# Kernel tuning notes

Hardware: AMD Instinct MI355X
Metric: run time of the kernel (lower is better)

## Reference

```python
import jax, jax.numpy as jnp
import numpy as np

NUM_EMBEDDINGS = 8192
EMBEDDING_DIM = 512
COMMITMENT_COST = 0.25
DECAY = 0.99
EPSILON = 1e-05


def setup_inputs() -> dict:
    key = jax.random.key(0)
    k1, k2, k3, k4 = jax.random.split(key, 4)
    z = jax.random.normal(k1, (16, 2048, EMBEDDING_DIM), dtype=jnp.float32)
    weight = jax.random.normal(k2, (NUM_EMBEDDINGS, EMBEDDING_DIM), dtype=jnp.float32)
    ema_cluster_size = jax.random.uniform(k3, (NUM_EMBEDDINGS,), dtype=jnp.float32)
    ema_w = jax.random.normal(k4, (NUM_EMBEDDINGS, EMBEDDING_DIM), dtype=jnp.float32)
    return {"z": z, "weight": weight, "ema_cluster_size": ema_cluster_size, "ema_w": ema_w}


def reference(z, weight, ema_cluster_size, ema_w):
    K, D = weight.shape
    z_flat = z.reshape(-1, D)                                   # [N, D]
    # squared-distance matrix via expanded GEMM (same math as torch)
    dist = ((z_flat ** 2).sum(1, keepdims=True)
            + (weight ** 2).sum(1)
            - 2.0 * z_flat @ weight.T)                          # [N, K]
    codes = jnp.argmin(dist, axis=1)                            # [N]
    # training-mode EMA update: one-hot sums expressed as segment_sum
    counts = jax.ops.segment_sum(jnp.ones(z_flat.shape[0], dtype=z.dtype), codes, num_segments=K)
    dw = jax.ops.segment_sum(z_flat, codes, num_segments=K)     # encodings.T @ z_flat
    new_cs = ema_cluster_size * DECAY + (1.0 - DECAY) * counts
    new_ema_w = ema_w * DECAY + (1.0 - DECAY) * dw
    n = new_cs.sum()
    cluster_size = (new_cs + EPSILON) / (n + K * EPSILON) * n
    new_weight = new_ema_w / cluster_size[:, None]              # updated codebook
    z_q = new_weight[codes].reshape(z.shape)                    # lookup with UPDATED weights
    vq_loss = COMMITMENT_COST * jnp.mean((jax.lax.stop_gradient(z_q) - z) ** 2)
    z_q_out = z + jax.lax.stop_gradient(z_q - z)                # straight-through estimator
    codes_out = codes.reshape(z.shape[0], -1)
    return vq_loss, z_q_out, codes_out, new_weight, new_cs, new_ema_w
```

## Files before the change

kernel.cpp:

```cpp
#include <hip/hip_runtime.h>
#include <cstdint>

#define K_CODES 8192
#define D_DIM   512
#define N_VEC   32768
#define DECAY   0.99f
#define EPS_VQ  1e-5f
#define COMMIT  0.25f
#define MARGIN  0.25f

typedef _Float16 half_t;
typedef _Float16 half8 __attribute__((ext_vector_type(8)));
typedef _Float16 half4 __attribute__((ext_vector_type(4)));
typedef float    f32x4 __attribute__((ext_vector_type(4)));
typedef unsigned long long u64;

#define GL2L(g, l)                                                              \
    __builtin_amdgcn_global_load_lds(                                           \
        (const __attribute__((address_space(1))) unsigned int*)(g),             \
        (__attribute__((address_space(3))) unsigned int*)(l), 16, 0, 0)

__device__ __forceinline__ unsigned ordf(float f) {
    unsigned u = __float_as_uint(f);
    return (u & 0x80000000u) ? ~u : (u | 0x80000000u);
}
__device__ __forceinline__ float unordf(unsigned u) {
    u = (u & 0x80000000u) ? (u & 0x7FFFFFFFu) : ~u;
    return __uint_as_float(u);
}


__global__ __launch_bounds__(256)
void conv_half_kernel(const float* __restrict__ x, half_t* __restrict__ out) {
    int i = blockIdx.x * 256 + threadIdx.x;
    float4 v = ((const float4*)x)[i];
    half4 h = { (_Float16)v.x, (_Float16)v.y, (_Float16)v.z, (_Float16)v.w };
    *(half4*)(out + (size_t)i * 4) = h;
}

__global__ __launch_bounds__(256)
void wsq_kernel(const float* __restrict__ w, float* __restrict__ wsq) {
    int wave = threadIdx.x >> 6, lane = threadIdx.x & 63;
    int row  = blockIdx.x * 4 + wave;
    const float4* p = (const float4*)(w + (size_t)row * D_DIM);
    float4 a = p[lane], b = p[lane + 64];
    float s = a.x*a.x + a.y*a.y + a.z*a.z + a.w*a.w
            + b.x*b.x + b.y*b.y + b.z*b.z + b.w*b.w;
    #pragma unroll
    for (int off = 32; off; off >>= 1) s += __shfl_down(s, off);
    if (lane == 0) wsq[row] = s;
}

__global__ __launch_bounds__(256, 4)
void dist1_kernel(const half_t* __restrict__ A, const half_t* __restrict__ B,
                  const float* __restrict__ wsq, uint4* __restrict__ partial) {
    __shared__ __align__(16) char smem[36864];
    half_t* As = (half_t*)smem;
    half_t* Bs = (half_t*)(smem + 16384);

    const int k0 = blockIdx.x * 128;
    const int n0 = blockIdx.y * 128;
    const int t    = threadIdx.x;
    const int lane = t & 63;
    const int wave = t >> 6;
    const int wm = (wave >> 1) * 64;
    const int wn = (wave & 1) * 64;
    const int l15 = lane & 15;
    const int q   = lane >> 4;

    const half_t* ga[4]; const half_t* gb[4]; half_t* lA[4]; half_t* lB[4];
    #pragma unroll
    for (int it = 0; it < 4; ++it) {
        int idx  = t + 256 * it;
        int row  = idx >> 3;
        int col8 = (idx & 7) ^ (row & 7);
        ga[it] = A + (size_t)(n0 + row) * D_DIM + col8 * 8;
        gb[it] = B + (size_t)(k0 + row) * D_DIM + col8 * 8;
        lA[it] = As + idx * 8;
        lB[it] = Bs + idx * 8;
    }

    f32x4 acc[4][4];
    #pragma unroll
    for (int mi = 0; mi < 4; ++mi)
        #pragma unroll
        for (int ni = 0; ni < 4; ++ni) acc[mi][ni] = (f32x4)0.0f;

    #pragma unroll
    for (int c = 0; c < 8; ++c) {
        #pragma unroll
        for (int it = 0; it < 4; ++it) {
            GL2L(ga[it] + c * 64, lA[it]);
            GL2L(gb[it] + c * 64, lB[it]);
        }
        __syncthreads();
        #pragma unroll
        for (int kk = 0; kk < 2; ++kk) {
            half8 af[4], bf[4];
            const int cpos = ((kk * 4 + q) ^ (l15 & 7)) * 8;
            #pragma unroll
            for (int mi = 0; mi < 4; ++mi)
                af[mi] = *(const half8*)&As[(wm + mi * 16 + l15) * 64 + cpos];
            #pragma unroll
            for (int ni = 0; ni < 4; ++ni)
                bf[ni] = *(const half8*)&Bs[(wn + ni * 16 + l15) * 64 + cpos];
            #pragma unroll
            for (int mi = 0; mi < 4; ++mi)
                #pragma unroll
                for (int ni = 0; ni < 4; ++ni)
                    acc[mi][ni] = __builtin_amdgcn_mfma_f32_16x16x32_f16(
                        af[mi], bf[ni], acc[mi][ni], 0, 0, 0);
        }
        __syncthreads();
    }

    uint2* kp  = (uint2*)(smem + wave * 8704);
    uint2* fmp = (uint2*)(smem + 34816);

    float wb[4]; unsigned cb[4];
    #pragma unroll
    for (int ni = 0; ni < 4; ++ni) {
        wb[ni] = 1024.0f - 0.5f * wsq[k0 + wn + ni * 16 + l15];
        cb[ni] = (unsigned)(wn + ni * 16 + l15);
    }

    #pragma unroll
    for (int mi = 0; mi < 4; ++mi) {
        #pragma unroll
        for (int r = 0; r < 4; ++r) {
            unsigned k1 = 0u, k2 = 0u;
            #pragma unroll
            for (int ni = 0; ni < 4; ++ni) {
                float a = acc[mi][ni][r] + wb[ni];
                unsigned key = (__float_as_uint(a) & 0xFFFFFF80u) | cb[ni];
                unsigned lo = min(k1, key);
                k1 = max(k1, key);
                k2 = max(k2, lo);
            }
            int row = mi * 16 + q * 4 + r;
            kp[row * 17 + l15] = make_uint2(k1, k2);
        }
    }
    __syncthreads();

    {
        const int rb = lane * 17;
        uint2 e0 = kp[rb];
        unsigned W1 = e0.x, W2 = e0.y;
        #pragma unroll
        for (int j = 1; j < 16; ++j) {
            uint2 e = kp[rb + j];
            unsigned lo = min(W1, e.x);
            W1 = max(W1, e.x);
            W2 = max(max(W2, lo), e.y);
        }
        fmp[(wave & 1) * 128 + wm + lane] = make_uint2(W1, W2);
    }
    __syncthreads();

    if (t < 128) {
        uint2 a = fmp[t], b = fmp[128 + t];
        unsigned W1 = max(a.x, b.x);
        unsigned W2 = max(max(min(a.x, b.x), a.y), b.y);
        unsigned col = (unsigned)k0 + (W1 & 127u);
        float v1 = __uint_as_float(W1 & 0xFFFFFF80u);
        float v2 = __uint_as_float(W2 & 0xFFFFFF80u);
        float d1 = 2048.0f - 2.0f * v1;
        float d2 = 2048.0f - 2.0f * v2;
        partial[(size_t)blockIdx.x * N_VEC + n0 + t] =
            make_uint4(col, ordf(d1), ordf(d2), 0u);
    }
}

__global__ __launch_bounds__(256)
void reduce_top2_kernel(const uint4* __restrict__ partial,
                        int* __restrict__ codes_i, float* __restrict__ codes_f,
                        int* __restrict__ cnt, int* __restrict__ list) {
    int row = blockIdx.x * 256 + threadIdx.x;
    u64 k1 = ~0ull, k2 = ~0ull;
    unsigned vm2 = 0xFFFFFFFFu;
    for (int kb = 0; kb < 64; ++kb) {
        uint4 e = partial[(size_t)kb * N_VEC + row];
        u64 k = ((u64)e.y << 32) | e.x;
        if (k < k1) { k2 = k1; k1 = k; }
        else if (k < k2) k2 = k;
        vm2 = min(vm2, e.z);
    }
    unsigned so = min((unsigned)(k2 >> 32), vm2);
    float bv = unordf((unsigned)(k1 >> 32));
    float sv = unordf(so);
    int code = (int)(k1 & 0xFFFFFFFFu);
    codes_i[row] = code;
    codes_f[row] = (float)code;
    if (sv - bv < MARGIN) { int p = atomicAdd(cnt, 1); list[p] = row; }
}

__global__ __launch_bounds__(256)
void refine2_kernel(const float* __restrict__ z, const float* __restrict__ w,
                    const float* __restrict__ wsq,
                    const int* __restrict__ cnt, const int* __restrict__ list,
                    u64* __restrict__ exact) {
    __shared__ float zs[64][68];
    __shared__ float ws[64][68];
    __shared__ int rows_s[64];
    const int n  = *cnt;
    const int c0 = blockIdx.x * 64;
    const int t  = threadIdx.x;
    const int lr = t & 63, lc = t >> 6;
    const int ty = t >> 4, tx = t & 15;

    for (int row0 = blockIdx.y * 64; row0 < n; row0 += gridDim.y * 64) {
        if (t < 64) {
            int ri = row0 + t;
            rows_s[t] = list[ri < n ? ri : n - 1];
        }
        __syncthreads();
        float acc[4][4] = {};
        const int zrow = rows_s[lr];
        for (int k0 = 0; k0 < D_DIM; k0 += 64) {
            #pragma unroll
            for (int it = 0; it < 4; ++it) {
                int kc = (lc * 4 + it) * 4;
                float4 v = *(const float4*)(z + (size_t)zrow * D_DIM + k0 + kc);
                zs[kc+0][lr] = v.x; zs[kc+1][lr] = v.y;
                zs[kc+2][lr] = v.z; zs[kc+3][lr] = v.w;
                float4 u = *(const float4*)(w + (size_t)(c0 + lr) * D_DIM + k0 + kc);
                ws[kc+0][lr] = u.x; ws[kc+1][lr] = u.y;
                ws[kc+2][lr] = u.z; ws[kc+3][lr] = u.w;
            }
            __syncthreads();
            #pragma unroll 8
            for (int k = 0; k < 64; ++k) {
                float4 za = *(const float4*)&zs[k][ty * 4];
                float4 wa = *(const float4*)&ws[k][tx * 4];
                float zav[4] = {za.x, za.y, za.z, za.w};
                float wav[4] = {wa.x, wa.y, wa.z, wa.w};
                #pragma unroll
                for (int i = 0; i < 4; ++i)
                    #pragma unroll
                    for (int j = 0; j < 4; ++j)
                        acc[i][j] += zav[i] * wav[j];
            }
            __syncthreads();
        }
        #pragma unroll
        for (int i = 0; i < 4; ++i) {
            u64 key = ~0ull;
            #pragma unroll
            for (int j = 0; j < 4; ++j) {
                int c = c0 + tx * 4 + j;
                float d = wsq[c] - 2.0f * acc[i][j];
                u64 k = ((u64)ordf(d) << 32) | (unsigned)c;
                if (k < key) key = k;
            }
            #pragma unroll
            for (int m = 1; m <= 8; m <<= 1) {
                u64 o = __shfl_xor(key, m);
                key = o < key ? o : key;
            }
            if (tx == 0) atomicMin(exact + rows_s[ty * 4 + i], key);
        }
        __syncthreads();
    }
}

__global__ __launch_bounds__(256)
void refine_fix_kernel(const int* __restrict__ cnt, const int* __restrict__ list,
                       const u64* __restrict__ exact,
                       int* __restrict__ codes_i, float* __restrict__ codes_f) {
    int n = *cnt;
    for (int i = blockIdx.x * 256 + threadIdx.x; i < n; i += 64 * 256) {
        int row = list[i];
        int code = (int)(exact[row] & 0xFFFFFFFFu);
        codes_i[row] = code;
        codes_f[row] = (float)code;
    }
}

__global__ __launch_bounds__(256)
void scatter_kernel(const int* __restrict__ codes_i, const float* __restrict__ z,
                    float* __restrict__ cnt_acc, float* __restrict__ dw_acc) {
    int row = blockIdx.x * 8 + (threadIdx.x >> 5);
    int c   = threadIdx.x & 31;
    int code = codes_i[row];
    if (c == 0) atomicAdd(&cnt_acc[code], 1.0f);
    const float* zr = z + (size_t)row * D_DIM;
    float* dr = dw_acc + (size_t)code * D_DIM;
    #pragma unroll
    for (int d = c; d < D_DIM; d += 32) atomicAdd(&dr[d], zr[d]);
}

__global__ __launch_bounds__(256)
void cs_kernel(const float* __restrict__ ema_cs, float* __restrict__ cs_out,
               float* __restrict__ nsum) {
    __shared__ float wsum[4];
    int i = blockIdx.x * 256 + threadIdx.x;
    float v = ema_cs[i] * DECAY + (1.0f - DECAY) * cs_out[i];
    cs_out[i] = v;
    float s = v;
    #pragma unroll
    for (int off = 32; off; off >>= 1) s += __shfl_down(s, off);
    int lane = threadIdx.x & 63, wid = threadIdx.x >> 6;
    if (lane == 0) wsum[wid] = s;
    __syncthreads();
    if (threadIdx.x == 0)
        atomicAdd(nsum, wsum[0] + wsum[1] + wsum[2] + wsum[3]);
}

__global__ __launch_bounds__(256)
void weight_kernel(const float* __restrict__ ema_w, const float* __restrict__ cs,
                   const float* __restrict__ nsum_p,
                   float* __restrict__ emaw_out, float* __restrict__ w_out) {
    int i = blockIdx.x * 256 + threadIdx.x;
    float dw = emaw_out[i];
    float ne = ema_w[i] * DECAY + (1.0f - DECAY) * dw;
    emaw_out[i] = ne;
    int k = i >> 9;
    float n = *nsum_p;
    float csize = (cs[k] + EPS_VQ) / (n + (float)K_CODES * EPS_VQ) * n;
    w_out[i] = ne / csize;
}

__global__ __launch_bounds__(256)
void gather_loss_kernel(const float* __restrict__ z, const int* __restrict__ codes,
                        const float* __restrict__ w, float* __restrict__ zq,
                        float* __restrict__ loss_acc) {
    __shared__ float wsum[4];
    int row  = blockIdx.x * 4 + (threadIdx.x >> 6);
    int lane = threadIdx.x & 63;
    int code = codes[row];
    const float* zr = z + (size_t)row * D_DIM;
    const float* wr = w + (size_t)code * D_DIM;
    float s = 0.0f;
    #pragma unroll
    for (int d = lane; d < D_DIM; d += 64) {
        float qv = wr[d];
        float diff = qv - zr[d];
        s += diff * diff;
        zq[(size_t)row * D_DIM + d] = qv;
    }
    #pragma unroll
    for (int off = 32; off; off >>= 1) s += __shfl_down(s, off);
    int wid = threadIdx.x >> 6;
    if (lane == 0) wsum[wid] = s;
    __syncthreads();
    if (threadIdx.x == 0)
        atomicAdd(loss_acc, wsum[0] + wsum[1] + wsum[2] + wsum[3]);
}

__global__ void finalize_kernel(const float* __restrict__ loss_acc,
                                float* __restrict__ out0) {
    *out0 = COMMIT * (*loss_acc) / 16777216.0f;
}

extern "C" void kernel_launch(void* const* d_in, const int* in_sizes, int n_in,
                              void* d_out, int out_size, void* d_ws, size_t ws_size,
                              hipStream_t stream) {
    const float* z      = (const float*)d_in[0];
    const float* weight = (const float*)d_in[1];
    const float* ema_cs = (const float*)d_in[2];
    const float* ema_w  = (const float*)d_in[3];

    float* out       = (float*)d_out;
    float* out_loss  = out;
    float* out_zq    = out + 1;
    float* out_codes = out + 16777217;
    float* out_w     = out + 16809985;
    float* out_cs    = out + 21004289;
    float* out_emaw  = out + 21012481;

    half_t* A_hi = (half_t*)(out + 4);
    half_t* B_hi = (half_t*)(out + 8388612);
    uint4*  partial = (uint4*)(out + 16809988);

    char* ws = (char*)d_ws;
    float* wsq      = (float*)ws;
    int*   codes_i  = (int*)(ws + 32768);
    int*   cnt      = (int*)(ws + 163840);
    float* nsum     = (float*)(ws + 163844);
    float* loss_acc = (float*)(ws + 163848);
    int*   list     = (int*)(ws + 163856);
    u64*   exact    = (u64*)(ws + 294928);

    hipMemsetAsync(cnt, 0, 16, stream);
    hipMemsetAsync(exact, 0xFF, N_VEC * 8, stream);

    conv_half_kernel<<<N_VEC * D_DIM / 1024, 256, 0, stream>>>(z, A_hi);
    conv_half_kernel<<<K_CODES * D_DIM / 1024, 256, 0, stream>>>(weight, B_hi);
    wsq_kernel<<<K_CODES / 4, 256, 0, stream>>>(weight, wsq);

    dim3 g2(K_CODES / 128, N_VEC / 128);
    dist1_kernel<<<g2, 256, 0, stream>>>(A_hi, B_hi, wsq, partial);

    reduce_top2_kernel<<<N_VEC / 256, 256, 0, stream>>>(partial, codes_i,
                                                        out_codes, cnt, list);

    hipMemsetAsync(out_cs, 0, 8192 * 4, stream);
    hipMemsetAsync(out_emaw, 0, (size_t)4194304 * 4, stream);

    dim3 gr(K_CODES / 64, 64);
    refine2_kernel<<<gr, 256, 0, stream>>>(z, weight, wsq, cnt, list, exact);
    refine_fix_kernel<<<64, 256, 0, stream>>>(cnt, list, exact,
                                              codes_i, out_codes);

    scatter_kernel<<<N_VEC / 8, 256, 0, stream>>>(codes_i, z, out_cs, out_emaw);
    cs_kernel<<<K_CODES / 256, 256, 0, stream>>>(ema_cs, out_cs, nsum);
    weight_kernel<<<4194304 / 256, 256, 0, stream>>>(ema_w, out_cs, nsum,
                                                     out_emaw, out_w);
    gather_loss_kernel<<<N_VEC / 4, 256, 0, stream>>>(z, codes_i, out_w,
                                                      out_zq, loss_acc);
    finalize_kernel<<<1, 1, 0, stream>>>(loss_acc, out_loss);
}
```

Before: 928.1 us.

## Enlarge distance GEMM tiles to 256x256 with double-buffered LDS and swizzle

The fp16 distance GEMM moves from 128x128 tiles with 4 waves to 256x256 tiles with 8 waves. It double-buffers global-to-LDS loads so the next K chunk streams in while the current one computes, remaps workgroups with an XCD-style swizzle, and raises MFMA priority. The larger tile halves the partial top-2 output, so the reduce loop now covers 32 blocks, and the key packing uses 8 index bits. The cost is 128 KB of LDS and heavier register use per block, which may limit occupancy or cause spills.

```diff
diff --git a/kernel.cpp b/kernel.cpp
--- a/kernel.cpp
+++ b/kernel.cpp
@@ -51,99 +51,120 @@
     if (lane == 0) wsq[row] = s;
 }
 
-__global__ __launch_bounds__(256, 4)
+__global__ __launch_bounds__(512, 2)
 void dist1_kernel(const half_t* __restrict__ A, const half_t* __restrict__ B,
                   const float* __restrict__ wsq, uint4* __restrict__ partial) {
-    __shared__ __align__(16) char smem[36864];
-    half_t* As = (half_t*)smem;
-    half_t* Bs = (half_t*)(smem + 16384);
-
-    const int k0 = blockIdx.x * 128;
-    const int n0 = blockIdx.y * 128;
+    __shared__ __align__(16) char smem[131072];
+    half_t* A0 = (half_t*)smem;
+    half_t* B0 = (half_t*)(smem + 32768);
+    half_t* A1 = (half_t*)(smem + 65536);
+    half_t* B1 = (half_t*)(smem + 98304);
+
+    const int wg  = blockIdx.x;
+    const int swz = (wg & 7) * 512 + (wg >> 3);
+    const int k0  = (swz & 31) * 256;
+    const int n0  = (swz >> 5) * 256;
+
     const int t    = threadIdx.x;
     const int lane = t & 63;
     const int wave = t >> 6;
-    const int wm = (wave >> 1) * 64;
-    const int wn = (wave & 1) * 64;
-    const int l15 = lane & 15;
-    const int q   = lane >> 4;
-
-    const half_t* ga[4]; const half_t* gb[4]; half_t* lA[4]; half_t* lB[4];
-    #pragma unroll
-    for (int it = 0; it < 4; ++it) {
-        int idx  = t + 256 * it;
+    const int wm   = (wave >> 2) * 128;
+    const int wn   = (wave & 3) * 64;
+    const int l15  = lane & 15;
+    const int q    = lane >> 4;
+
+    const half_t* ga[4]; const half_t* gb[4];
+    #pragma unroll
+    for (int i = 0; i < 4; ++i) {
+        int idx  = t + 512 * i;
         int row  = idx >> 3;
         int col8 = (idx & 7) ^ (row & 7);
-        ga[it] = A + (size_t)(n0 + row) * D_DIM + col8 * 8;
-        gb[it] = B + (size_t)(k0 + row) * D_DIM + col8 * 8;
-        lA[it] = As + idx * 8;
-        lB[it] = Bs + idx * 8;
-    }
-
-    f32x4 acc[4][4];
-    #pragma unroll
-    for (int mi = 0; mi < 4; ++mi)
+        ga[i] = A + (size_t)(n0 + row) * D_DIM + col8 * 8;
+        gb[i] = B + (size_t)(k0 + row) * D_DIM + col8 * 8;
+    }
+
+    f32x4 acc[8][4];
+    #pragma unroll
+    for (int mi = 0; mi < 8; ++mi)
         #pragma unroll
         for (int ni = 0; ni < 4; ++ni) acc[mi][ni] = (f32x4)0.0f;
 
-    #pragma unroll
-    for (int c = 0; c < 8; ++c) {
-        #pragma unroll
-        for (int it = 0; it < 4; ++it) {
-            GL2L(ga[it] + c * 64, lA[it]);
-            GL2L(gb[it] + c * 64, lB[it]);
-        }
-        __syncthreads();
+    auto stage = [&](int kt, half_t* la, half_t* lb) {
+        #pragma unroll
+        for (int i = 0; i < 4; ++i) {
+            GL2L(ga[i] + kt * 64, la + (size_t)(t + 512 * i) * 8);
+            GL2L(gb[i] + kt * 64, lb + (size_t)(t + 512 * i) * 8);
+        }
+    };
+    auto compute = [&](const half_t* la, const half_t* lb) {
         #pragma unroll
         for (int kk = 0; kk < 2; ++kk) {
-            half8 af[4], bf[4];
+            half8 af[8], bf[4];
             const int cpos = ((kk * 4 + q) ^ (l15 & 7)) * 8;
             #pragma unroll
-            for (int mi = 0; mi < 4; ++mi)
-                af[mi] = *(const half8*)&As[(wm + mi * 16 + l15) * 64 + cpos];
+            for (int mi = 0; mi < 8; ++mi)
+                af[mi] = *(const half8*)&la[(wm + mi * 16 + l15) * 64 + cpos];
             #pragma unroll
             for (int ni = 0; ni < 4; ++ni)
-                bf[ni] = *(const half8*)&Bs[(wn + ni * 16 + l15) * 64 + cpos];
-            #pragma unroll
-            for (int mi = 0; mi < 4; ++mi)
+                bf[ni] = *(const half8*)&lb[(wn + ni * 16 + l15) * 64 + cpos];
+            __builtin_amdgcn_s_setprio(1);
+            #pragma unroll
+            for (int mi = 0; mi < 8; ++mi)
                 #pragma unroll
                 for (int ni = 0; ni < 4; ++ni)
                     acc[mi][ni] = __builtin_amdgcn_mfma_f32_16x16x32_f16(
                         af[mi], bf[ni], acc[mi][ni], 0, 0, 0);
-        }
-        __syncthreads();
+            __builtin_amdgcn_s_setprio(0);
+        }
+    };
+
+    stage(0, A0, B0);
+    #pragma unroll
+    for (int kt = 0; kt < 8; ++kt) {
+        half_t* la = (kt & 1) ? A1 : A0;
+        half_t* lb = (kt & 1) ? B1 : B0;
+        if (kt < 7) {
+            stage(kt + 1, (kt & 1) ? A0 : A1, (kt & 1) ? B0 : B1);
+            asm volatile("s_waitcnt vmcnt(8)" ::: "memory");
+        } else {
+            asm volatile("s_waitcnt vmcnt(0)" ::: "memory");
+        }
+        __builtin_amdgcn_s_barrier();
+        compute(la, lb);
+        __builtin_amdgcn_s_barrier();
     }
 
     uint2* kp  = (uint2*)(smem + wave * 8704);
-    uint2* fmp = (uint2*)(smem + 34816);
+    uint2* fmp = (uint2*)(smem + 69632);
 
     float wb[4]; unsigned cb[4];
     #pragma unroll
     for (int ni = 0; ni < 4; ++ni) {
-        wb[ni] = 1024.0f - 0.5f * wsq[k0 + wn + ni * 16 + l15];
+        wb[ni] = 512.0f - 0.5f * wsq[k0 + wn + ni * 16 + l15];
         cb[ni] = (unsigned)(wn + ni * 16 + l15);
     }
 
-    #pragma unroll
-    for (int mi = 0; mi < 4; ++mi) {
-        #pragma unroll
-        for (int r = 0; r < 4; ++r) {
-            unsigned k1 = 0u, k2 = 0u;
-            #pragma unroll
-            for (int ni = 0; ni < 4; ++ni) {
-                float a = acc[mi][ni][r] + wb[ni];
-                unsigned key = (__float_as_uint(a) & 0xFFFFFF80u) | cb[ni];
-                unsigned lo = min(k1, key);
-                k1 = max(k1, key);
-                k2 = max(k2, lo);
+    uint2 res[2];
+    #pragma unroll
+    for (int half = 0; half < 2; ++half) {
+        #pragma unroll
+        for (int mi2 = 0; mi2 < 4; ++mi2) {
+            const int mi = half * 4 + mi2;
+            #pragma unroll
+            for (int r = 0; r < 4; ++r) {
+                unsigned k1 = 0u, k2 = 0u;
+                #pragma unroll
+                for (int ni = 0; ni < 4; ++ni) {
+                    float a = acc[mi][ni][r] + wb[ni];
+                    unsigned key = (__float_as_uint(a) & 0xFFFFFF00u) | cb[ni];
+                    unsigned lo = min(k1, key);
+                    k1 = max(k1, key);
+                    k2 = max(k2, lo);
+                }
+                int row = mi2 * 16 + q * 4 + r;
+                kp[row * 17 + l15] = make_uint2(k1, k2);
             }
-            int row = mi * 16 + q * 4 + r;
-            kp[row * 17 + l15] = make_uint2(k1, k2);
-        }
-    }
-    __syncthreads();
-
-    {
+        }
         const int rb = lane * 17;
         uint2 e0 = kp[rb];
         unsigned W1 = e0.x, W2 = e0.y;
@@ -154,20 +175,27 @@
             W1 = max(W1, e.x);
             W2 = max(max(W2, lo), e.y);
         }
-        fmp[(wave & 1) * 128 + wm + lane] = make_uint2(W1, W2);
-    }
-    __syncthreads();
-
-    if (t < 128) {
-        uint2 a = fmp[t], b = fmp[128 + t];
-        unsigned W1 = max(a.x, b.x);
-        unsigned W2 = max(max(min(a.x, b.x), a.y), b.y);
-        unsigned col = (unsigned)k0 + (W1 & 127u);
-        float v1 = __uint_as_float(W1 & 0xFFFFFF80u);
-        float v2 = __uint_as_float(W2 & 0xFFFFFF80u);
-        float d1 = 2048.0f - 2.0f * v1;
-        float d2 = 2048.0f - 2.0f * v2;
-        partial[(size_t)blockIdx.x * N_VEC + n0 + t] =
+        res[half] = make_uint2(W1, W2);
+    }
+    fmp[(wm + lane) * 4 + (wave & 3)]      = res[0];
+    fmp[(wm + 64 + lane) * 4 + (wave & 3)] = res[1];
+    asm volatile("s_waitcnt lgkmcnt(0)" ::: "memory");
+    __builtin_amdgcn_s_barrier();
+
+    if (t < 256) {
+        uint2 a = fmp[t * 4 + 0], b = fmp[t * 4 + 1];
+        uint2 c = fmp[t * 4 + 2], d = fmp[t * 4 + 3];
+        unsigned mab = max(a.x, b.x), mcd = max(c.x, d.x);
+        unsigned sab = min(a.x, b.x), scd = min(c.x, d.x);
+        unsigned W1 = max(mab, mcd);
+        unsigned sec1 = max(min(mab, mcd), max(sab, scd));
+        unsigned W2 = max(max(max(a.y, b.y), max(c.y, d.y)), sec1);
+        unsigned col = (unsigned)k0 + (W1 & 255u);
+        float v1 = __uint_as_float(W1 & 0xFFFFFF00u);
+        float v2 = __uint_as_float(W2 & 0xFFFFFF00u);
+        float d1 = 1024.0f - 2.0f * v1;
+        float d2 = 1024.0f - 2.0f * v2;
+        partial[(size_t)(swz & 31) * N_VEC + n0 + t] =
             make_uint4(col, ordf(d1), ordf(d2), 0u);
     }
 }
@@ -179,7 +207,7 @@
     int row = blockIdx.x * 256 + threadIdx.x;
     u64 k1 = ~0ull, k2 = ~0ull;
     unsigned vm2 = 0xFFFFFFFFu;
-    for (int kb = 0; kb < 64; ++kb) {
+    for (int kb = 0; kb < 32; ++kb) {
         uint4 e = partial[(size_t)kb * N_VEC + row];
         u64 k = ((u64)e.y << 32) | e.x;
         if (k < k1) { k2 = k1; k1 = k; }
@@ -389,8 +417,7 @@
     conv_half_kernel<<<K_CODES * D_DIM / 1024, 256, 0, stream>>>(weight, B_hi);
     wsq_kernel<<<K_CODES / 4, 256, 0, stream>>>(weight, wsq);
 
-    dim3 g2(K_CODES / 128, N_VEC / 128);
-    dist1_kernel<<<g2, 256, 0, stream>>>(A_hi, B_hi, wsq, partial);
+    dist1_kernel<<<4096, 512, 0, stream>>>(A_hi, B_hi, wsq, partial);
 
     reduce_top2_kernel<<<N_VEC / 256, 256, 0, stream>>>(partial, codes_i,
                                                         out_codes, cnt, list);
```

Result: no change. 918.7 us (-1.0%).
